# Performance work log

Hardware: AMD Instinct MI355X
Metric: run time of the kernel (lower is better)

Reference implementation:

```python
import jax, jax.numpy as jnp
import numpy as np

WINDOW_SIZE = 11
SIGMA = 1.5
C1 = 0.01 ** 2
C2 = 0.03 ** 2
ALPHA = 0.84


def _gaussian_window(window_size, sigma):
    x = np.arange(window_size, dtype=np.float32)
    g = np.exp(-((x - window_size // 2) ** 2) / (2.0 * sigma ** 2))
    g = g / g.sum()
    w2d = np.outer(g, g).astype(np.float32)  # [K, K]
    return jnp.asarray(w2d)


def _depthwise_conv(x, window):
    # x: [B, C, H, W]; window: [K, K] shared across channels (depthwise)
    C = x.shape[1]
    K = window.shape[0]
    kern = jnp.broadcast_to(window[None, None], (C, 1, K, K))  # [C, 1, K, K] OIHW
    pad = K // 2
    return jax.lax.conv_general_dilated(
        x, kern,
        window_strides=(1, 1),
        padding=((pad, pad), (pad, pad)),
        dimension_numbers=('NCHW', 'OIHW', 'NCHW'),
        feature_group_count=C,
    )


def _ssim(img1, img2):
    window = _gaussian_window(WINDOW_SIZE, SIGMA)
    mu1 = _depthwise_conv(img1, window)
    mu2 = _depthwise_conv(img2, window)
    mu1_sq = mu1 * mu1
    mu2_sq = mu2 * mu2
    mu1_mu2 = mu1 * mu2
    sigma1_sq = _depthwise_conv(img1 * img1, window) - mu1_sq
    sigma2_sq = _depthwise_conv(img2 * img2, window) - mu2_sq
    sigma12 = _depthwise_conv(img1 * img2, window) - mu1_mu2
    ssim_map = ((2 * mu1_mu2 + C1) * (2 * sigma12 + C2)) / (
        (mu1_sq + mu2_sq + C1) * (sigma1_sq + sigma2_sq + C2))
    return ssim_map.mean()


def setup_inputs() -> dict:
    key = jax.random.key(0)
    k1, k2 = jax.random.split(key)
    shape = (32, 3, 512, 512)
    pred = jax.random.uniform(k1, shape, dtype=jnp.float32)
    target = jax.random.uniform(k2, shape, dtype=jnp.float32)
    return {"pred": pred, "target": target}


def reference(pred, target):
    l1 = jnp.mean(jnp.abs(pred - target))
    s = _ssim(pred, target)
    return ALPHA * l1 + (1.0 - ALPHA) * (1.0 - s)
```

## Files before the change

### kernel.cpp

```cpp
#include <hip/hip_runtime.h>

#define SSIM_H 512
#define SSIM_W 512
#define PLANES 96
#define TILE_W 64
#define TILE_H 32
#define GRID_X (SSIM_W / TILE_W)
#define GRID_Y (SSIM_H / TILE_H)
#define TOTAL_BLOCKS (GRID_X * GRID_Y * PLANES)
#define N_TOTAL 25165824.0

#define RAW_ROWS 44
#define RAW_STRIDE 86
#define RAW_CHUNKS (2 * RAW_ROWS * 21)
#define STG_FULL (RAW_CHUNKS / 256)
#define STG_TAIL (RAW_CHUNKS - STG_FULL * 256)

typedef _Float16 half4v __attribute__((ext_vector_type(4)));
typedef _Float16 half8v __attribute__((ext_vector_type(8)));
typedef float float4v __attribute__((ext_vector_type(4)));

struct __align__(8) f2 { float x, y; };

__device__ __forceinline__ float gwf(int k) {
  const float d = (float)(k - 5);
  return __expf(-d * d / 4.5f) * 0.26601171702936207f;
}

__global__ __launch_bounds__(256, 3)
void ssim_l1_kernel(const float* __restrict__ pred,
                    const float* __restrict__ targ,
                    f2* __restrict__ partials) {
  __shared__ float Raw[2][RAW_ROWS][RAW_STRIDE];
  __shared__ _Float16 Hs[4][64][44];
  __shared__ float red[2][4];

  const int tid = (int)threadIdx.x;
  const int wv = tid >> 6;
  const int lane = tid & 63;
  const int q = lane >> 4;
  const int m = lane & 15;

  const int tr0 = (int)blockIdx.y * TILE_H;
  const int tc0 = (int)blockIdx.x * TILE_W;
  const size_t pbase = (size_t)blockIdx.z * (SSIM_H * SSIM_W);
  const float* __restrict__ xp = pred + pbase;
  const float* __restrict__ yp = targ + pbase;

  float4v stg[8];
  int doff[8];
#pragma unroll
  for (int k = 0; k < 8; ++k) {
    if (k < STG_FULL || tid < STG_TAIL) {
      const int c = k * 256 + tid;
      const int row = c / 42;
      const int rem = c - row * 42;
      const int img = rem / 21;
      const int pos = rem - img * 21;
      const int gr = min(max(tr0 - 5 + row, 0), SSIM_H - 1);
      const int gc = min(max(tc0 - 8 + 4 * pos, 0), SSIM_W - 4);
      const float* src = (img ? yp : xp) + ((size_t)gr << 9) + gc;
      asm volatile("global_load_dwordx4 %0, %1, off"
                   : "=v"(stg[k]) : "v"(src) : "memory");
      doff[k] = (img * RAW_ROWS + row) * RAW_STRIDE + 4 * pos;
    }
  }
  asm volatile("s_waitcnt vmcnt(0)" ::: "memory");
  __builtin_amdgcn_sched_barrier(0);
#pragma unroll
  for (int k = 0; k < 8; ++k) {
    if (k < STG_FULL || tid < STG_TAIL) {
      float* d = &Raw[0][0][0] + doff[k];
      f2 lo, hi;
      lo.x = stg[k][0]; lo.y = stg[k][1];
      hi.x = stg[k][2]; hi.y = stg[k][3];
      *(f2*)d = lo;
      *(f2*)(d + 2) = hi;
    }
  }
  __syncthreads();

  half8v wf;
#pragma unroll
  for (int j = 0; j < 8; ++j) {
    const int k = 8 * q + j - m;
    const float v = (k >= 0 && k <= 10) ? gwf(k) : 0.0f;
    wf[j] = (_Float16)v;
  }

  const int cw = tc0 + 16 * wv;
  const int cbase = cw - 5 + 8 * q;
  const int o = 16 * wv + 8 * q + 3;
  const bool xedge = (tc0 == 0) || (tc0 == SSIM_W - TILE_W);
  const bool yedge = (tr0 == 0) || (tr0 == SSIM_H - TILE_H);

  float l1 = 0.0f;

#pragma unroll
  for (int rg = 0; rg < 3; ++rg) {
    const int r = rg * 16 + m;
    const int rs = r < 43 ? r : 43;
    const float* Rx = &Raw[0][rs][0];
    const float* Ry = &Raw[1][rs][0];
    f2 a0 = *(const f2*)(Rx + o - 1);
    f2 a1 = *(const f2*)(Rx + o + 1);
    f2 a2 = *(const f2*)(Rx + o + 3);
    f2 a3 = *(const f2*)(Rx + o + 5);
    float a4 = Rx[o + 7];
    f2 b0 = *(const f2*)(Ry + o - 1);
    f2 b1 = *(const f2*)(Ry + o + 1);
    f2 b2 = *(const f2*)(Ry + o + 3);
    f2 b3 = *(const f2*)(Ry + o + 5);
    float b4 = Ry[o + 7];
    float xf[8] = {a0.y, a1.x, a1.y, a2.x, a2.y, a3.x, a3.y, a4};
    float yf[8] = {b0.y, b1.x, b1.y, b2.x, b2.y, b3.x, b3.y, b4};

    if (yedge) {
      const bool okr = (unsigned)(tr0 - 5 + r) < (unsigned)SSIM_H;
#pragma unroll
      for (int j = 0; j < 8; ++j) {
        xf[j] = okr ? xf[j] : 0.0f;
        yf[j] = okr ? yf[j] : 0.0f;
      }
    }
    if (xedge) {
#pragma unroll
      for (int j = 0; j < 8; ++j) {
        const bool ok = (unsigned)(cbase + j) < (unsigned)SSIM_W;
        xf[j] = ok ? xf[j] : 0.0f;
        yf[j] = ok ? yf[j] : 0.0f;
      }
    }

    if (r >= 5 && r < 5 + TILE_H) {
#pragma unroll
      for (int j = 0; j < 8; ++j) {
        const int k = 8 * q + j;
        if (k >= 5 && k < 21) l1 += fabsf(xf[j] - yf[j]);
      }
    }

    half8v ax, ay, axxyy, axy;
#pragma unroll
    for (int j = 0; j < 8; ++j) {
      const float x = xf[j], y = yf[j];
      ax[j]    = (_Float16)x;
      ay[j]    = (_Float16)y;
      axxyy[j] = (_Float16)(x * x + y * y);
      axy[j]   = (_Float16)(x * y);
    }
    const float4v z = {0.0f, 0.0f, 0.0f, 0.0f};
    float4v c0 = __builtin_amdgcn_mfma_f32_16x16x32_f16(ax,    wf, z, 0, 0, 0);
    float4v c1 = __builtin_amdgcn_mfma_f32_16x16x32_f16(ay,    wf, z, 0, 0, 0);
    float4v c2 = __builtin_amdgcn_mfma_f32_16x16x32_f16(axxyy, wf, z, 0, 0, 0);
    float4v c3 = __builtin_amdgcn_mfma_f32_16x16x32_f16(axy,   wf, z, 0, 0, 0);

    if (rg != 2 || q != 3) {
      const int hcol = 16 * wv + m;
      const int hrow = rg * 16 + 4 * q;
      half4v h;
      h[0] = (_Float16)c0[0]; h[1] = (_Float16)c0[1];
      h[2] = (_Float16)c0[2]; h[3] = (_Float16)c0[3];
      *(half4v*)&Hs[0][hcol][hrow] = h;
      h[0] = (_Float16)c1[0]; h[1] = (_Float16)c1[1];
      h[2] = (_Float16)c1[2]; h[3] = (_Float16)c1[3];
      *(half4v*)&Hs[1][hcol][hrow] = h;
      h[0] = (_Float16)c2[0]; h[1] = (_Float16)c2[1];
      h[2] = (_Float16)c2[2]; h[3] = (_Float16)c2[3];
      *(half4v*)&Hs[2][hcol][hrow] = h;
      h[0] = (_Float16)c3[0]; h[1] = (_Float16)c3[1];
      h[2] = (_Float16)c3[2]; h[3] = (_Float16)c3[3];
      *(half4v*)&Hs[3][hcol][hrow] = h;
    }
  }

  asm volatile("s_waitcnt lgkmcnt(0)" ::: "memory");
  __builtin_amdgcn_sched_barrier(0);

  float ssim = 0.0f;
  {
    const int hcol = 16 * wv + m;
    half8v bfr[2][4];
#pragma unroll
    for (int rb = 0; rb < 2; ++rb) {
      const int hrow = 16 * rb + 8 * q;
      const int hrow_hi = (hrow + 4 <= 40) ? hrow + 4 : 40;
#pragma unroll
      for (int p = 0; p < 4; ++p) {
        half4v lo = *(const half4v*)&Hs[p][hcol][hrow];
        half4v hi = *(const half4v*)&Hs[p][hcol][hrow_hi];
        bfr[rb][p] = __builtin_shufflevector(lo, hi, 0, 1, 2, 3, 4, 5, 6, 7);
      }
    }
    const float C1v = 1.0e-4f, C2v = 9.0e-4f;
#pragma unroll
    for (int rb = 0; rb < 2; ++rb) {
      const float4v z = {0.0f, 0.0f, 0.0f, 0.0f};
      float4v acc[4];
#pragma unroll
      for (int p = 0; p < 4; ++p)
        acc[p] = __builtin_amdgcn_mfma_f32_16x16x32_f16(wf, bfr[rb][p], z,
                                                        0, 0, 0);
#pragma unroll
      for (int r = 0; r < 4; ++r) {
        const float mu1 = acc[0][r], mu2 = acc[1][r];
        const float exxyy = acc[2][r], exy = acc[3][r];
        const float m11 = mu1 * mu1, m22 = mu2 * mu2, m12 = mu1 * mu2;
        const float num = (2.0f * m12 + C1v) * (2.0f * (exy - m12) + C2v);
        const float den = (m11 + m22 + C1v) *
                          ((exxyy - m11 - m22) + C2v);
        ssim += num / den;
      }
    }
  }

  float v0 = l1, v1 = ssim;
#pragma unroll
  for (int off = 32; off > 0; off >>= 1) {
    v0 += __shfl_down(v0, off, 64);
    v1 += __shfl_down(v1, off, 64);
  }
  if (lane == 0) { red[0][wv] = v0; red[1][wv] = v1; }
  __syncthreads();
  if (tid == 0) {
    f2 s;
    s.x = red[0][0] + red[0][1] + red[0][2] + red[0][3];
    s.y = red[1][0] + red[1][1] + red[1][2] + red[1][3];
    const int bid = ((int)blockIdx.z * GRID_Y + (int)blockIdx.y) * GRID_X +
                    (int)blockIdx.x;
    partials[bid] = s;
  }
}

__global__ __launch_bounds__(256)
void finalize_kernel(const f2* __restrict__ partials,
                     float* __restrict__ out) {
  __shared__ double red[2][4];
  const int tid = (int)threadIdx.x;
  double L = 0.0, S = 0.0;
  for (int i = tid; i < TOTAL_BLOCKS; i += 256) {
    const f2 v = partials[i];
    L += (double)v.x;
    S += (double)v.y;
  }
#pragma unroll
  for (int off = 32; off > 0; off >>= 1) {
    L += __shfl_down(L, off, 64);
    S += __shfl_down(S, off, 64);
  }
  const int lane = tid & 63, wid = tid >> 6;
  if (lane == 0) { red[0][wid] = L; red[1][wid] = S; }
  __syncthreads();
  if (tid == 0) {
    const double Ls = red[0][0] + red[0][1] + red[0][2] + red[0][3];
    const double Ss = red[1][0] + red[1][1] + red[1][2] + red[1][3];
    const double invN = 1.0 / N_TOTAL;
    out[0] = (float)(0.84 * (Ls * invN) + 0.16 * (1.0 - Ss * invN));
  }
}

extern "C" void kernel_launch(void* const* d_in, const int* in_sizes, int n_in,
                              void* d_out, int out_size, void* d_ws, size_t ws_size,
                              hipStream_t stream) {
  const float* pred = (const float*)d_in[0];
  const float* targ = (const float*)d_in[1];
  float* out = (float*)d_out;
  f2* partials = (f2*)d_ws;

  dim3 grid(GRID_X, GRID_Y, PLANES);
  ssim_l1_kernel<<<grid, 256, 0, stream>>>(pred, targ, partials);
  finalize_kernel<<<1, 256, 0, stream>>>(partials, out);
}
```

Baseline: 262.3 us.

## Load input tiles directly into LDS via global_load_lds with edge patching

Replaces the register-staged global loads and LDS stores with direct global-to-LDS loads (global_load_lds, 16 bytes per lane), using a contiguous 90-float row layout that matches the wave-linear LDS write pattern. Edge tiles receive a small patch write to fix the clamped columns. It also computes the squared and cross products in packed fp16 instead of fp32, which cuts VALU work but lowers precision of the second-moment inputs. The aim is to free staging VGPRs and remove the separate LDS write pass, at the cost of more complex index maths and a risk of LDS bank conflicts from the unpadded stride.

```diff
diff --git a/kernel.cpp b/kernel.cpp
--- a/kernel.cpp
+++ b/kernel.cpp
@@ -10,11 +10,8 @@
 #define TOTAL_BLOCKS (GRID_X * GRID_Y * PLANES)
 #define N_TOTAL 25165824.0
 
-#define RAW_ROWS 44
-#define RAW_STRIDE 86
-#define RAW_CHUNKS (2 * RAW_ROWS * 21)
-#define STG_FULL (RAW_CHUNKS / 256)
-#define STG_TAIL (RAW_CHUNKS - STG_FULL * 256)
+#define RAW_DW_IMG 3960
+#define RAW_CHUNKS 1980
 
 typedef _Float16 half4v __attribute__((ext_vector_type(4)));
 typedef _Float16 half8v __attribute__((ext_vector_type(8)));
@@ -31,7 +28,7 @@
 void ssim_l1_kernel(const float* __restrict__ pred,
                     const float* __restrict__ targ,
                     f2* __restrict__ partials) {
-  __shared__ float Raw[2][RAW_ROWS][RAW_STRIDE];
+  __shared__ unsigned int RawU[2 * RAW_DW_IMG];
   __shared__ _Float16 Hs[4][64][44];
   __shared__ float red[2][4];
 
@@ -47,38 +44,42 @@
   const float* __restrict__ xp = pred + pbase;
   const float* __restrict__ yp = targ + pbase;
 
-  float4v stg[8];
-  int doff[8];
 #pragma unroll
   for (int k = 0; k < 8; ++k) {
-    if (k < STG_FULL || tid < STG_TAIL) {
-      const int c = k * 256 + tid;
-      const int row = c / 42;
-      const int rem = c - row * 42;
-      const int img = rem / 21;
-      const int pos = rem - img * 21;
-      const int gr = min(max(tr0 - 5 + row, 0), SSIM_H - 1);
-      const int gc = min(max(tc0 - 8 + 4 * pos, 0), SSIM_W - 4);
+    const int c = k * 256 + tid;
+    if (c < RAW_CHUNKS) {
+      const int img = (c >= 990);
+      const int cc = c - (img ? 990 : 0);
+      const int t = cc << 2;
+      const int r = (int)(((unsigned)t * 46604u) >> 22);
+      const int w = t - 90 * r;
+      int gr = tr0 - 5 + r;
+      gr = gr < 0 ? 0 : (gr > 511 ? 511 : gr);
+      int gc = w + (tc0 - 10);
+      gc = gc < 0 ? 0 : (gc > 508 ? 508 : gc);
       const float* src = (img ? yp : xp) + ((size_t)gr << 9) + gc;
-      asm volatile("global_load_dwordx4 %0, %1, off"
-                   : "=v"(stg[k]) : "v"(src) : "memory");
-      doff[k] = (img * RAW_ROWS + row) * RAW_STRIDE + 4 * pos;
-    }
-  }
-  asm volatile("s_waitcnt vmcnt(0)" ::: "memory");
-  __builtin_amdgcn_sched_barrier(0);
-#pragma unroll
-  for (int k = 0; k < 8; ++k) {
-    if (k < STG_FULL || tid < STG_TAIL) {
-      float* d = &Raw[0][0][0] + doff[k];
-      f2 lo, hi;
-      lo.x = stg[k][0]; lo.y = stg[k][1];
-      hi.x = stg[k][2]; hi.y = stg[k][3];
-      *(f2*)d = lo;
-      *(f2*)(d + 2) = hi;
-    }
-  }
-  __syncthreads();
+      __builtin_amdgcn_global_load_lds(
+          (const __attribute__((address_space(1))) unsigned int*)src,
+          (__attribute__((address_space(3))) unsigned int*)
+              ((char*)RawU + (k << 12) + ((tid >> 6) << 10)),
+          16, 0, 0);
+    }
+  }
+
+  const bool xl = (tc0 == 0), xr = (tc0 == SSIM_W - TILE_W);
+  f2 patch;
+  bool dop = false;
+  int pD = 0;
+  if ((xl | xr) && tid < 88) {
+    dop = true;
+    const int pim = tid >= 44;
+    const int r = tid - (pim ? 44 : 0);
+    int gr = tr0 - 5 + r;
+    gr = gr < 0 ? 0 : (gr > 511 ? 511 : gr);
+    const int cL = xl ? 0 : 510;
+    patch = *(const f2*)((pim ? yp : xp) + ((size_t)gr << 9) + cL);
+    pD = pim * RAW_DW_IMG + 90 * r + 2 + (cL - (tc0 - 8));
+  }
 
   half8v wf;
 #pragma unroll
@@ -88,30 +89,33 @@
     wf[j] = (_Float16)v;
   }
 
+  asm volatile("s_waitcnt vmcnt(0)" ::: "memory");
+  if (dop) *(f2*)&RawU[pD] = patch;
+  __syncthreads();
+
   const int cw = tc0 + 16 * wv;
   const int cbase = cw - 5 + 8 * q;
-  const int o = 16 * wv + 8 * q + 3;
-  const bool xedge = (tc0 == 0) || (tc0 == SSIM_W - TILE_W);
   const bool yedge = (tr0 == 0) || (tr0 == SSIM_H - TILE_H);
 
   float l1 = 0.0f;
 
+  const int Bbase = 16 * wv + 8 * q + 4;
 #pragma unroll
   for (int rg = 0; rg < 3; ++rg) {
     const int r = rg * 16 + m;
     const int rs = r < 43 ? r : 43;
-    const float* Rx = &Raw[0][rs][0];
-    const float* Ry = &Raw[1][rs][0];
-    f2 a0 = *(const f2*)(Rx + o - 1);
-    f2 a1 = *(const f2*)(Rx + o + 1);
-    f2 a2 = *(const f2*)(Rx + o + 3);
-    f2 a3 = *(const f2*)(Rx + o + 5);
-    float a4 = Rx[o + 7];
-    f2 b0 = *(const f2*)(Ry + o - 1);
-    f2 b1 = *(const f2*)(Ry + o + 1);
-    f2 b2 = *(const f2*)(Ry + o + 3);
-    f2 b3 = *(const f2*)(Ry + o + 5);
-    float b4 = Ry[o + 7];
+    const float* Rx = (const float*)RawU + 90 * rs + Bbase;
+    const float* Ry = Rx + RAW_DW_IMG;
+    f2 a0 = *(const f2*)Rx;
+    f2 a1 = *(const f2*)(Rx + 2);
+    f2 a2 = *(const f2*)(Rx + 4);
+    f2 a3 = *(const f2*)(Rx + 6);
+    float a4 = Rx[8];
+    f2 b0 = *(const f2*)Ry;
+    f2 b1 = *(const f2*)(Ry + 2);
+    f2 b2 = *(const f2*)(Ry + 4);
+    f2 b3 = *(const f2*)(Ry + 6);
+    float b4 = Ry[8];
     float xf[8] = {a0.y, a1.x, a1.y, a2.x, a2.y, a3.x, a3.y, a4};
     float yf[8] = {b0.y, b1.x, b1.y, b2.x, b2.y, b3.x, b3.y, b4};
 
@@ -123,7 +127,7 @@
         yf[j] = okr ? yf[j] : 0.0f;
       }
     }
-    if (xedge) {
+    if (xl | xr) {
 #pragma unroll
       for (int j = 0; j < 8; ++j) {
         const bool ok = (unsigned)(cbase + j) < (unsigned)SSIM_W;
@@ -140,15 +144,15 @@
       }
     }
 
-    half8v ax, ay, axxyy, axy;
+    half8v ax, ay;
 #pragma unroll
     for (int j = 0; j < 8; ++j) {
-      const float x = xf[j], y = yf[j];
-      ax[j]    = (_Float16)x;
-      ay[j]    = (_Float16)y;
-      axxyy[j] = (_Float16)(x * x + y * y);
-      axy[j]   = (_Float16)(x * y);
-    }
+      ax[j] = (_Float16)xf[j];
+      ay[j] = (_Float16)yf[j];
+    }
+    half8v axxyy = ax * ax + ay * ay;
+    half8v axy = ax * ay;
+
     const float4v z = {0.0f, 0.0f, 0.0f, 0.0f};
     float4v c0 = __builtin_amdgcn_mfma_f32_16x16x32_f16(ax,    wf, z, 0, 0, 0);
     float4v c1 = __builtin_amdgcn_mfma_f32_16x16x32_f16(ay,    wf, z, 0, 0, 0);
```

Result: no change. 263.9 us (+0.6%).
